# Performance work log

Hardware: AMD Instinct MI355X
Metric: run time of the kernel (lower is better)

## Reference

```python
import jax, jax.numpy as jnp
from jax import lax
import numpy as np

B, L, H = 2048, 2048, 64
DP_DIM, EPS_DIM = 4, 1
IN_DIM = DP_DIM + EPS_DIM + 1  # 6, per docstring


def setup_inputs() -> dict:
    key = jax.random.key(0)
    ks = jax.random.split(key, 13)
    s = 1.0 / np.sqrt(H)
    u = lambda k, shape: jax.random.uniform(k, shape, jnp.float32, -s, s)
    return {
        "dP": jax.random.normal(ks[0], (B, L, DP_DIM), jnp.float32),
        "eps": jax.random.normal(ks[1], (B, L, EPS_DIM), jnp.float32),
        "W_ih0": u(ks[2], (4 * H, IN_DIM)), "W_hh0": u(ks[3], (4 * H, H)),
        "b_ih0": u(ks[4], (4 * H,)), "b_hh0": u(ks[5], (4 * H,)),
        "W_ih1": u(ks[6], (4 * H, H)), "W_hh1": u(ks[7], (4 * H, H)),
        "b_ih1": u(ks[8], (4 * H,)), "b_hh1": u(ks[9], (4 * H,)),
        "W_head": u(ks[10], (1, H)), "b_head": u(ks[11], (1,)),
        "lengths": jax.random.randint(ks[12], (B,), 1, L + 1),
        "reverse": 0,
    }


def _lstm_cell(x, h, c, W_ih, W_hh, b_ih, b_hh):
    # PyTorch LSTMCell gate layout: i, f, g, o
    g = x @ W_ih.T + b_ih + h @ W_hh.T + b_hh
    i, f, gg, o = jnp.split(g, 4, axis=-1)
    c_new = jax.nn.sigmoid(f) * c + jax.nn.sigmoid(i) * jnp.tanh(gg)
    h_new = jax.nn.sigmoid(o) * jnp.tanh(c_new)
    return h_new, c_new


def _forward(dP, eps, W_ih0, W_hh0, b_ih0, b_hh0, W_ih1, W_hh1, b_ih1, b_hh1,
             W_head, b_head, lengths, reverse):
    Bsz, Ln, _ = dP.shape
    Hd = W_hh0.shape[1]
    x_all = jnp.concatenate([dP, eps], axis=-1).transpose(1, 0, 2)  # (L,B,5)
    t_vals = jnp.arange(Ln)
    if reverse:
        x_all = x_all[::-1]
        t_vals = t_vals[::-1]

    h_d0 = jnp.zeros((Bsz, 1), dP.dtype)
    hs0 = jnp.zeros((2, Bsz, Hd), dP.dtype)
    cs0 = jnp.zeros((2, Bsz, Hd), dP.dtype)

    def step(carry, inp):
        h_d, hs, cs = carry
        x5, t = inp
        active = (t < lengths)[:, None]  # (B,1) bool
        x = jnp.concatenate([x5, h_d], axis=-1)  # (B,6)
        h0, c0 = _lstm_cell(x, hs[0], cs[0], W_ih0, W_hh0, b_ih0, b_hh0)
        h1, c1 = _lstm_cell(h0, hs[1], cs[1], W_ih1, W_hh1, b_ih1, b_hh1)
        delta = h1 @ W_head.T + b_head  # (B,1)
        h_prev = h_d
        h_d_new = jnp.where(active, h_d + delta, h_d)
        # inactive rows have their LSTM state zeroed (matches torch.where(..., zero))
        new_hs = jnp.where(active[None], jnp.stack([h0, h1]), jnp.zeros_like(hs))
        new_cs = jnp.where(active[None], jnp.stack([c0, c1]), jnp.zeros_like(cs))
        return (h_d_new, new_hs, new_cs), (h_prev, delta)

    _, (h_seq, d_seq) = lax.scan(step, (h_d0, hs0, cs0), (x_all, t_vals))
    h_seq = h_seq.transpose(1, 0, 2)  # (B,L,1) in iteration order
    d_seq = d_seq.transpose(1, 0, 2)
    if reverse:
        h_seq = h_seq[:, ::-1]
        d_seq = d_seq[:, ::-1]
    return h_seq, d_seq


def reference(dP, eps, W_ih0, W_hh0, b_ih0, b_hh0, W_ih1, W_hh1, b_ih1, b_hh1,
              W_head, b_head, lengths, reverse):
    return _forward(dP, eps, W_ih0, W_hh0, b_ih0, b_hh0, W_ih1, W_hh1,
                    b_ih1, b_hh1, W_head, b_head, lengths, reverse)
```

## Files before the change

kernel.cpp:

```cpp
#include <hip/hip_runtime.h>
#include <hip/hip_bf16.h>

#define B_TOT 2048
#define L_SEQ 2048
#define NBLK  256
#define BQ    8
#define NWAVE 8
#define XBS   328

typedef __attribute__((ext_vector_type(8))) short bf16x8;
typedef __attribute__((ext_vector_type(4))) float f32x4;

#if __has_builtin(__builtin_amdgcn_exp2f)
static __device__ __forceinline__ float fexp2(float x){ return __builtin_amdgcn_exp2f(x); }
#else
static __device__ __forceinline__ float fexp2(float x){ return exp2f(x); }
#endif
#if __has_builtin(__builtin_amdgcn_rcpf)
static __device__ __forceinline__ float frcp (float x){ return __builtin_amdgcn_rcpf(x); }
#else
static __device__ __forceinline__ float frcp (float x){ return 1.0f / x; }
#endif

static __device__ __forceinline__ unsigned short f2bf(float f){
  union { float f; unsigned int u; } v; v.f = f;
  unsigned int u = v.u;
  u += 0x7FFFu + ((u >> 16) & 1u);
  return (unsigned short)(u >> 16);
}
static __device__ __forceinline__ unsigned int cvtpk(float a, float b){
  unsigned int r;
  asm("v_cvt_pk_bf16_f32 %0, %1, %2" : "=v"(r) : "v"(a), "v"(b));
  return r;
}

static __device__ __forceinline__ float sigm_pre(float x, float bpre){
  return frcp(1.f + fexp2(__builtin_fmaf(x, -1.4426950408889634f, bpre)));
}
static __device__ __forceinline__ float tanh_pre(float x, float bpre){
  return 1.f - 2.f*frcp(1.f + fexp2(__builtin_fmaf(x, 2.8853900817779268f, bpre)));
}
static __device__ __forceinline__ float cell_act(float gi,float gf,float gg,float go,
    float bi,float bf,float bg,float bo, float& c, bool act){
  float is = sigm_pre(gi, bi);
  float fs = sigm_pre(gf, bf);
  float gt = tanh_pre(gg, bg);
  float os = sigm_pre(go, bo);
  float cn = __builtin_fmaf(fs, c, is*gt);
  float h  = os * tanh_pre(cn, 0.f);
  c = act ? cn : 0.f;
  return h;
}

#define STEP(PAR, TCUR)                                                         \
  {                                                                             \
    const int  t_   = (TCUR);                                                   \
    const int  tp_  = rev ? (L_SEQ-1-t_) : t_;                                  \
    const bool act_ = tp_ < lenb;                                               \
    const bool ap_  = (t_ == 0) || ((rev ? (L_SEQ - t_) : (t_-1)) < lenb);      \
    f32x4 a0a={0,0,0,0}, a0b={0,0,0,0}, a1a={0,0,0,0}, a1b={0,0,0,0};           \
    {                                                                           \
      const unsigned short* pzz = &ZZb[0];                                      \
      const unsigned short* pk0 = ap_ ? (Brow + 64*((PAR)^1)       + 8*g) : pzz;\
      const unsigned short* pk1 = ap_ ? (Brow + 64*((PAR)^1) + 32  + 8*g) : pzz;\
      const unsigned short* ph2 = ap_ ? (Brow + 128 + 64*((PAR)^1)      + 8*g) : pzz;\
      const unsigned short* ph3 = ap_ ? (Brow + 128 + 64*((PAR)^1) + 32 + 8*g) : pzz;\
      bf16x8 bk0 = *(const bf16x8*)pk0;                                         \
      bf16x8 bk1 = *(const bf16x8*)pk1;                                         \
      bf16x8 bx  = *(const bf16x8*)(Brow + 256 + 32*(PAR) + 8*g);               \
      bf16x8 bh2 = *(const bf16x8*)ph2;                                         \
      bf16x8 bh3 = *(const bf16x8*)ph3;                                         \
      a0a = __builtin_amdgcn_mfma_f32_16x16x32_bf16(A0[0][0], bk0, a0a,0,0,0);  \
      a0b = __builtin_amdgcn_mfma_f32_16x16x32_bf16(A0[1][0], bk0, a0b,0,0,0);  \
      a0a = __builtin_amdgcn_mfma_f32_16x16x32_bf16(A0[0][1], bk1, a0a,0,0,0);  \
      a0b = __builtin_amdgcn_mfma_f32_16x16x32_bf16(A0[1][1], bk1, a0b,0,0,0);  \
      a0a = __builtin_amdgcn_mfma_f32_16x16x32_bf16(A0[0][2], bx,  a0a,0,0,0);  \
      a0b = __builtin_amdgcn_mfma_f32_16x16x32_bf16(A0[1][2], bx,  a0b,0,0,0);  \
      a1a = __builtin_amdgcn_mfma_f32_16x16x32_bf16(A1[0][2], bh2, a1a,0,0,0);  \
      a1b = __builtin_amdgcn_mfma_f32_16x16x32_bf16(A1[1][2], bh2, a1b,0,0,0);  \
      a1a = __builtin_amdgcn_mfma_f32_16x16x32_bf16(A1[0][3], bh3, a1a,0,0,0);  \
      a1b = __builtin_amdgcn_mfma_f32_16x16x32_bf16(A1[1][3], bh3, a1b,0,0,0);  \
    }                                                                           \
    {                                                                           \
      float h0v = cell_act(__builtin_fmaf(wx[0][0],h_d,a0a[0]),                 \
                           __builtin_fmaf(wx[1][0],h_d,a0a[1]),                 \
                           __builtin_fmaf(wx[2][0],h_d,a0b[0]),                 \
                           __builtin_fmaf(wx[3][0],h_d,a0b[1]),                 \
                           bp0[0][0],bp0[1][0],bp0[2][0],bp0[3][0], c00, act_); \
      float h1v = cell_act(__builtin_fmaf(wx[0][1],h_d,a0a[2]),                 \
                           __builtin_fmaf(wx[1][1],h_d,a0a[3]),                 \
                           __builtin_fmaf(wx[2][1],h_d,a0b[2]),                 \
                           __builtin_fmaf(wx[3][1],h_d,a0b[3]),                 \
                           bp0[0][1],bp0[1][1],bp0[2][1],bp0[3][1], c01, act_); \
      *(unsigned int*)&XB[r16][64*(PAR) + 8*w + 2*g] = cvtpk(h0v, h1v);         \
      if (xload){                                                               \
        unsigned int* dst = (unsigned int*)&XB[l][256 + 32*((PAR)^1)];          \
        dst[0] = cvtpk(xr0, xr1);                                               \
        dst[1] = cvtpk(xr2, xr3);                                               \
        XB[l][256 + 32*((PAR)^1) + 4] = (unsigned short)cvtpk(xr4, xr4);        \
        int ts = t_ + 2;                                                        \
        int tpn = rev ? (L_SEQ-1-ts) : ts;                                      \
        tpn = tpn < 0 ? 0 : (tpn >= L_SEQ ? L_SEQ-1 : tpn);                     \
        const float4 v_ = *(const float4*)(dP + ((size_t)(b0+l)*L_SEQ + tpn)*4);\
        xr0=v_.x; xr1=v_.y; xr2=v_.z; xr3=v_.w;                                 \
        xr4 = eps[(size_t)(b0+l)*L_SEQ + tpn];                                  \
      }                                                                         \
    }                                                                           \
    __syncthreads();                        \
    {                                                                           \
      bf16x8 bk0 = *(const bf16x8*)(Brow + 64*(PAR)      + 8*g);                \
      bf16x8 bk1 = *(const bf16x8*)(Brow + 64*(PAR) + 32 + 8*g);                \
      a1a = __builtin_amdgcn_mfma_f32_16x16x32_bf16(A1[0][0], bk0, a1a,0,0,0);  \
      a1b = __builtin_amdgcn_mfma_f32_16x16x32_bf16(A1[1][0], bk0, a1b,0,0,0);  \
      a1a = __builtin_amdgcn_mfma_f32_16x16x32_bf16(A1[0][1], bk1, a1a,0,0,0);  \
      a1b = __builtin_amdgcn_mfma_f32_16x16x32_bf16(A1[1][1], bk1, a1b,0,0,0);  \
    }                                                                           \
    {                                                                           \
      if (l < 16) dpart[(PAR)^1][l] = 0.f;     \
      float h0v = cell_act(a1a[0],a1a[1],a1b[0],a1b[1],                         \
                           bp1[0][0],bp1[1][0],bp1[2][0],bp1[3][0], c10, act_); \
      float h1v = cell_act(a1a[2],a1a[3],a1b[2],a1b[3],                         \
                           bp1[0][1],bp1[1][1],bp1[2][1],bp1[3][1], c11, act_); \
      *(unsigned int*)&XB[r16][128 + 64*(PAR) + 8*w + 2*g] = cvtpk(h0v, h1v);   \
      float s_ = __builtin_fmaf(wh0, h0v, wh1*h1v);                             \
      s_ += __shfl_xor(s_, 16, 64);                                             \
      s_ += __shfl_xor(s_, 32, 64);                                             \
      if (l < 16) atomicAdd(&dpart[(PAR)][l], s_);                              \
    }                                                                           \
    __syncthreads();                        \
    {                                                                           \
      const float dsum_ = bhead + dpart[(PAR)][r16];                            \
      const float hp_ = h_d;                                                    \
      if (act_) h_d += dsum_;                                                   \
      if (w == 0 && l < 8){                                                     \
        out[(size_t)(b0+l)*L_SEQ + tp_] = hp_;                                  \
        out[(size_t)B_TOT*L_SEQ + (size_t)(b0+l)*L_SEQ + tp_] = dsum_;          \
      }                                                                         \
    }                                                                           \
  }

__global__ __launch_bounds__(512, 2)
void dh_lstm(const float* __restrict__ dP, const float* __restrict__ eps,
             const float* __restrict__ Wih0, const float* __restrict__ Whh0,
             const float* __restrict__ bih0, const float* __restrict__ bhh0,
             const float* __restrict__ Wih1, const float* __restrict__ Whh1,
             const float* __restrict__ bih1, const float* __restrict__ bhh1,
             const float* __restrict__ Whead, const float* __restrict__ bhead_p,
             const int* __restrict__ lengths, const int* __restrict__ revp,
             float* __restrict__ out)
{
  __shared__ unsigned short XB[16][XBS];
  __shared__ float dpart[2][16];
  __shared__ __align__(16) unsigned short ZZb[16];

  const int tid = threadIdx.x;
  const int l   = tid & 63;
  const int w   = tid >> 6;
  const int g   = l >> 4;
  const int r16 = l & 15;
  const int b0  = blockIdx.x * BQ;
  const int rev = revp[0];

  {
    unsigned int* p = (unsigned int*)&XB[0][0];
    for (int i = tid; i < 16*XBS/2; i += 512) p[i] = 0u;
    if (tid < 32) ((float*)dpart)[tid] = 0.f;
    if (tid < 16) ZZb[tid] = 0;
  }

  bf16x8 A0[2][3], A1[2][4];
  {
    const int u  = r16 >> 1;
    const int t0 = r16 & 1;
#pragma unroll
    for (int tau = 0; tau < 2; ++tau){
      const int j = 64*(2*tau + t0) + 8*w + u;
#pragma unroll
      for (int k = 0; k < 3; ++k){
        bf16x8 a;
#pragma unroll
        for (int e = 0; e < 8; ++e){
          const int c = 32*k + 8*g + e;
          float v = 0.f;
          if (c < 64) v = Whh0[j*64 + c];
          else if (c < 70) v = Wih0[j*6 + (c-64)];
          a[e] = (short)f2bf(v);
        }
        A0[tau][k] = a;
      }
#pragma unroll
      for (int k = 0; k < 4; ++k){
        bf16x8 a;
#pragma unroll
        for (int e = 0; e < 8; ++e){
          const int c = 32*k + 8*g + e;
          const float v = (c < 64) ? Wih1[j*64 + c] : Whh1[j*64 + (c-64)];
          a[e] = (short)f2bf(v);
        }
        A1[tau][k] = a;
      }
    }
  }

  float bp0[4][2], bp1[4][2], wx[4][2];
#pragma unroll
  for (int t4 = 0; t4 < 4; ++t4){
#pragma unroll
    for (int j = 0; j < 2; ++j){
      const int jj = 64*t4 + 8*w + 2*g + j;
      const float sc = (t4 == 2) ? 2.8853900817779268f : -1.4426950408889634f;
      bp0[t4][j] = sc * (bih0[jj] + bhh0[jj]);
      bp1[t4][j] = sc * (bih1[jj] + bhh1[jj]);
      wx[t4][j]  = Wih0[jj*6 + 5];
    }
  }
  const float wh0 = Whead[8*w + 2*g + 0];
  const float wh1 = Whead[8*w + 2*g + 1];
  const float bhead = bhead_p[0];
  const int   lenb  = lengths[b0 + (r16 & 7)];

  __syncthreads();

  float xr0=0,xr1=0,xr2=0,xr3=0,xr4=0;
  const bool xload = (w == 1) && (l < 8);
  if (xload){
    const int t0p = rev ? (L_SEQ-1) : 0;
    const float4 v = *(const float4*)(dP + ((size_t)(b0+l)*L_SEQ + t0p)*4);
    const float ev = eps[(size_t)(b0+l)*L_SEQ + t0p];
    unsigned int* dst = (unsigned int*)&XB[l][256];
    dst[0] = cvtpk(v.x, v.y);
    dst[1] = cvtpk(v.z, v.w);
    XB[l][256+4] = (unsigned short)cvtpk(ev, ev);
    const int t1p = rev ? (L_SEQ-2) : 1;
    const float4 v1 = *(const float4*)(dP + ((size_t)(b0+l)*L_SEQ + t1p)*4);
    xr0=v1.x; xr1=v1.y; xr2=v1.z; xr3=v1.w;
    xr4 = eps[(size_t)(b0+l)*L_SEQ + t1p];
  }
  __syncthreads();

  float c00=0,c01=0,c10=0,c11=0, h_d=0;
  const unsigned short* Brow = &XB[r16][0];

#pragma unroll 1
  for (int t2 = 0; t2 < L_SEQ; t2 += 2){
    STEP(0, t2)
    STEP(1, t2 + 1)
  }
}

extern "C" void kernel_launch(void* const* d_in, const int* in_sizes, int n_in,
                              void* d_out, int out_size, void* d_ws, size_t ws_size,
                              hipStream_t stream) {
  (void)in_sizes; (void)n_in; (void)d_ws; (void)ws_size; (void)out_size;
  dh_lstm<<<dim3(NBLK), dim3(512), 0, stream>>>(
      (const float*)d_in[0],  (const float*)d_in[1],
      (const float*)d_in[2],  (const float*)d_in[3],
      (const float*)d_in[4],  (const float*)d_in[5],
      (const float*)d_in[6],  (const float*)d_in[7],
      (const float*)d_in[8],  (const float*)d_in[9],
      (const float*)d_in[10], (const float*)d_in[11],
      (const int*)d_in[12],   (const int*)d_in[13],
      (float*)d_out);
}
```

Baseline: 2.377 ms.

## Halve batch rows per block and remap MFMA gate rows for one cell per lane

Each block now handles 4 sequences instead of 8, so twice as many blocks launch, with launch bounds raised to allow 4 blocks per CU. The weight-row mapping is reordered so the four gates of one hidden unit land in one lane, or in its xor-4 partner, which is fetched with a shuffle. Each lane then evaluates one LSTM cell instead of two. The head reduction replaces shared atomics with per-wave partial sums that are summed after the barrier. The MFMA N dimension stays 16 with only 4 real batch columns, so matrix work per sequence doubles, which is traded for more parallelism across the serial time loop.

```diff
diff --git a/kernel.cpp b/kernel.cpp
--- a/kernel.cpp
+++ b/kernel.cpp
@@ -3,8 +3,8 @@
 
 #define B_TOT 2048
 #define L_SEQ 2048
-#define NBLK  256
-#define BQ    8
+#define NBLK  512
+#define BQ    4
 #define NWAVE 8
 #define XBS   328
 
@@ -61,8 +61,8 @@
     f32x4 a0a={0,0,0,0}, a0b={0,0,0,0}, a1a={0,0,0,0}, a1b={0,0,0,0};           \
     {                                                                           \
       const unsigned short* pzz = &ZZb[0];                                      \
-      const unsigned short* pk0 = ap_ ? (Brow + 64*((PAR)^1)       + 8*g) : pzz;\
-      const unsigned short* pk1 = ap_ ? (Brow + 64*((PAR)^1) + 32  + 8*g) : pzz;\
+      const unsigned short* pk0 = ap_ ? (Brow + 64*((PAR)^1)            + 8*g) : pzz;\
+      const unsigned short* pk1 = ap_ ? (Brow + 64*((PAR)^1)       + 32 + 8*g) : pzz;\
       const unsigned short* ph2 = ap_ ? (Brow + 128 + 64*((PAR)^1)      + 8*g) : pzz;\
       const unsigned short* ph3 = ap_ ? (Brow + 128 + 64*((PAR)^1) + 32 + 8*g) : pzz;\
       bf16x8 bk0 = *(const bf16x8*)pk0;                                         \
@@ -81,18 +81,23 @@
       a1a = __builtin_amdgcn_mfma_f32_16x16x32_bf16(A1[0][3], bh3, a1a,0,0,0);  \
       a1b = __builtin_amdgcn_mfma_f32_16x16x32_bf16(A1[1][3], bh3, a1b,0,0,0);  \
     }                                                                           \
-    {                                                                           \
-      float h0v = cell_act(__builtin_fmaf(wx[0][0],h_d,a0a[0]),                 \
-                           __builtin_fmaf(wx[1][0],h_d,a0a[1]),                 \
-                           __builtin_fmaf(wx[2][0],h_d,a0b[0]),                 \
-                           __builtin_fmaf(wx[3][0],h_d,a0b[1]),                 \
-                           bp0[0][0],bp0[1][0],bp0[2][0],bp0[3][0], c00, act_); \
-      float h1v = cell_act(__builtin_fmaf(wx[0][1],h_d,a0a[2]),                 \
-                           __builtin_fmaf(wx[1][1],h_d,a0a[3]),                 \
-                           __builtin_fmaf(wx[2][1],h_d,a0b[2]),                 \
-                           __builtin_fmaf(wx[3][1],h_d,a0b[3]),                 \
-                           bp0[0][1],bp0[1][1],bp0[2][1],bp0[3][1], c01, act_); \
-      *(unsigned int*)&XB[r16][64*(PAR) + 8*w + 2*g] = cvtpk(h0v, h1v);         \
+    {                      \
+      const float xi = __shfl_xor(a0b[0], 4, 64);                               \
+      const float xf = __shfl_xor(a0b[1], 4, 64);                               \
+      const float xg = __shfl_xor(a0b[2], 4, 64);                               \
+      const float xo = __shfl_xor(a0b[3], 4, 64);                               \
+      float gi = hb ? xi : a0a[0];                                              \
+      float gf = hb ? xf : a0a[1];                                              \
+      float gg = hb ? xg : a0a[2];                                              \
+      float go = hb ? xo : a0a[3];                                              \
+      gi = __builtin_fmaf(wxv[0], h_d, gi);                                     \
+      gf = __builtin_fmaf(wxv[1], h_d, gf);                                     \
+      gg = __builtin_fmaf(wxv[2], h_d, gg);                                     \
+      go = __builtin_fmaf(wxv[3], h_d, go);                                     \
+      const float h0v = cell_act(gi,gf,gg,go,                                   \
+                                 bp0v[0],bp0v[1],bp0v[2],bp0v[3], c0s, act_);   \
+      if (r16 < 8)                                                              \
+        XB[b4][64*(PAR) + ju] = (unsigned short)cvtpk(h0v, h0v);                \
       if (xload){                                                               \
         unsigned int* dst = (unsigned int*)&XB[l][256 + 32*((PAR)^1)];          \
         dst[0] = cvtpk(xr0, xr1);                                               \
@@ -115,31 +120,40 @@
       a1a = __builtin_amdgcn_mfma_f32_16x16x32_bf16(A1[0][1], bk1, a1a,0,0,0);  \
       a1b = __builtin_amdgcn_mfma_f32_16x16x32_bf16(A1[1][1], bk1, a1b,0,0,0);  \
     }                                                                           \
-    {                                                                           \
-      if (l < 16) dpart[(PAR)^1][l] = 0.f;     \
-      float h0v = cell_act(a1a[0],a1a[1],a1b[0],a1b[1],                         \
-                           bp1[0][0],bp1[1][0],bp1[2][0],bp1[3][0], c10, act_); \
-      float h1v = cell_act(a1a[2],a1a[3],a1b[2],a1b[3],                         \
-                           bp1[0][1],bp1[1][1],bp1[2][1],bp1[3][1], c11, act_); \
-      *(unsigned int*)&XB[r16][128 + 64*(PAR) + 8*w + 2*g] = cvtpk(h0v, h1v);   \
-      float s_ = __builtin_fmaf(wh0, h0v, wh1*h1v);                             \
+    {             \
+      const float xi = __shfl_xor(a1b[0], 4, 64);                               \
+      const float xf = __shfl_xor(a1b[1], 4, 64);                               \
+      const float xg = __shfl_xor(a1b[2], 4, 64);                               \
+      const float xo = __shfl_xor(a1b[3], 4, 64);                               \
+      const float gi = hb ? xi : a1a[0];                                        \
+      const float gf = hb ? xf : a1a[1];                                        \
+      const float gg = hb ? xg : a1a[2];                                        \
+      const float go = hb ? xo : a1a[3];                                        \
+      const float h1v = cell_act(gi,gf,gg,go,                                   \
+                                 bp1v[0],bp1v[1],bp1v[2],bp1v[3], c1s, act_);   \
+      if (r16 < 8)                                                              \
+        XB[b4][128 + 64*(PAR) + ju] = (unsigned short)cvtpk(h1v, h1v);          \
+      float s_ = wh * h1v;                                                      \
+      s_ += __shfl_xor(s_, 4, 64);                                              \
       s_ += __shfl_xor(s_, 16, 64);                                             \
       s_ += __shfl_xor(s_, 32, 64);                                             \
-      if (l < 16) atomicAdd(&dpart[(PAR)][l], s_);                              \
-    }                                                                           \
-    __syncthreads();                        \
+      if (l < 4) dpart[w][l] = s_;                                              \
+    }                                                                           \
+    __syncthreads();                             \
     {                                                                           \
-      const float dsum_ = bhead + dpart[(PAR)][r16];                            \
+      float dsum_ = bhead;                                                      \
+      _Pragma("unroll")                                                         \
+      for (int ww = 0; ww < NWAVE; ++ww) dsum_ += dpart[ww][b4];                \
       const float hp_ = h_d;                                                    \
       if (act_) h_d += dsum_;                                                   \
-      if (w == 0 && l < 8){                                                     \
+      if (w == 0 && l < 4){                                                     \
         out[(size_t)(b0+l)*L_SEQ + tp_] = hp_;                                  \
         out[(size_t)B_TOT*L_SEQ + (size_t)(b0+l)*L_SEQ + tp_] = dsum_;          \
       }                                                                         \
     }                                                                           \
   }
 
-__global__ __launch_bounds__(512, 2)
+__global__ __launch_bounds__(512, 4)
 void dh_lstm(const float* __restrict__ dP, const float* __restrict__ eps,
              const float* __restrict__ Wih0, const float* __restrict__ Whh0,
              const float* __restrict__ bih0, const float* __restrict__ bhh0,
@@ -150,7 +164,7 @@
              float* __restrict__ out)
 {
   __shared__ unsigned short XB[16][XBS];
-  __shared__ float dpart[2][16];
+  __shared__ float dpart[NWAVE][16];
   __shared__ __align__(16) unsigned short ZZb[16];
 
   const int tid = threadIdx.x;
@@ -158,23 +172,25 @@
   const int w   = tid >> 6;
   const int g   = l >> 4;
   const int r16 = l & 15;
+  const int b4  = r16 & 3;
+  const int hb  = (r16 >> 2) & 1;
   const int b0  = blockIdx.x * BQ;
   const int rev = revp[0];
 
   {
     unsigned int* p = (unsigned int*)&XB[0][0];
     for (int i = tid; i < 16*XBS/2; i += 512) p[i] = 0u;
-    if (tid < 32) ((float*)dpart)[tid] = 0.f;
+    if (tid < NWAVE*16) ((float*)dpart)[tid] = 0.f;
     if (tid < 16) ZZb[tid] = 0;
   }
 
   bf16x8 A0[2][3], A1[2][4];
   {
-    const int u  = r16 >> 1;
-    const int t0 = r16 & 1;
+    const int gate = r16 & 3;
+    const int uo   = r16 >> 2;
 #pragma unroll
     for (int tau = 0; tau < 2; ++tau){
-      const int j = 64*(2*tau + t0) + 8*w + u;
+      const int j = 64*gate + 8*w + 4*tau + uo;
 #pragma unroll
       for (int k = 0; k < 3; ++k){
         bf16x8 a;
@@ -202,27 +218,24 @@
     }
   }
 
-  float bp0[4][2], bp1[4][2], wx[4][2];
+  const int ju = 8*w + 4*hb + g;
+  float bp0v[4], bp1v[4], wxv[4];
 #pragma unroll
   for (int t4 = 0; t4 < 4; ++t4){
-#pragma unroll
-    for (int j = 0; j < 2; ++j){
-      const int jj = 64*t4 + 8*w + 2*g + j;
-      const float sc = (t4 == 2) ? 2.8853900817779268f : -1.4426950408889634f;
-      bp0[t4][j] = sc * (bih0[jj] + bhh0[jj]);
-      bp1[t4][j] = sc * (bih1[jj] + bhh1[jj]);
-      wx[t4][j]  = Wih0[jj*6 + 5];
-    }
-  }
-  const float wh0 = Whead[8*w + 2*g + 0];
-  const float wh1 = Whead[8*w + 2*g + 1];
+    const int jj = 64*t4 + ju;
+    const float sc = (t4 == 2) ? 2.8853900817779268f : -1.4426950408889634f;
+    bp0v[t4] = sc * (bih0[jj] + bhh0[jj]);
+    bp1v[t4] = sc * (bih1[jj] + bhh1[jj]);
+    wxv[t4]  = Wih0[jj*6 + 5];
+  }
+  const float wh    = Whead[ju];
   const float bhead = bhead_p[0];
-  const int   lenb  = lengths[b0 + (r16 & 7)];
+  const int   lenb  = lengths[b0 + b4];
 
   __syncthreads();
 
   float xr0=0,xr1=0,xr2=0,xr3=0,xr4=0;
-  const bool xload = (w == 1) && (l < 8);
+  const bool xload = (w == 1) && (l < 4);
   if (xload){
     const int t0p = rev ? (L_SEQ-1) : 0;
     const float4 v = *(const float4*)(dP + ((size_t)(b0+l)*L_SEQ + t0p)*4);
@@ -238,7 +251,7 @@
   }
   __syncthreads();
 
-  float c00=0,c01=0,c10=0,c11=0, h_d=0;
+  float c0s=0.f, c1s=0.f, h_d=0.f;
   const unsigned short* Brow = &XB[r16][0];
 
 #pragma unroll 1
```

Result: slower. 2.932 ms (+23.3%).
